# Kernel tuning notes

Hardware: AMD Instinct MI355X
Metric: run time of the kernel (lower is better)

The kernel has to match this reference:

```python
import jax, jax.numpy as jnp
import numpy as np

BN_EPS = 1e-5
CLAMP = 1e-4


def setup_inputs() -> dict:
    key = jax.random.key(0)
    ks = jax.random.split(key, 13)
    B, C, T, A = 32, 1536, 1000, 128
    s = 0.02  # keep conv pre-activations in a sane range
    return {
        "x": jax.random.normal(ks[0], (B, C, T), jnp.float32),
        "W1": jax.random.normal(ks[1], (A, 3 * C), jnp.float32) * s,
        "b1": jax.random.normal(ks[2], (A,), jnp.float32) * s,
        "g1": jax.random.uniform(ks[3], (A,), jnp.float32, 0.5, 1.5),
        "beta1": jax.random.normal(ks[4], (A,), jnp.float32) * 0.1,
        "rm1": jax.random.normal(ks[5], (A,), jnp.float32) * 0.1,
        "rv1": jax.random.uniform(ks[6], (A,), jnp.float32, 0.5, 1.5),
        "W2": jax.random.normal(ks[7], (C, A), jnp.float32) * s,
        "b2": jax.random.normal(ks[8], (C,), jnp.float32) * s,
        "g2": jax.random.uniform(ks[9], (C,), jnp.float32, 0.5, 1.5),
        "beta2": jax.random.normal(ks[10], (C,), jnp.float32) * 0.1,
        "rm2": jax.random.normal(ks[11], (C,), jnp.float32) * 0.1,
        "rv2": jax.random.uniform(ks[12], (C,), jnp.float32, 0.5, 1.5),
    }


def _bn(h, g, beta, rm, rv):
    # inference-mode BatchNorm1d over channel axis 1 of [B, C, T]
    inv = g / jnp.sqrt(rv + BN_EPS)
    return h * inv[None, :, None] + (beta - rm * inv)[None, :, None]


def reference(x, W1, b1, g1, beta1, rm1, rv1, W2, b2, g2, beta2, rm2, rv2):
    B, C, T = x.shape
    mean = jnp.mean(x, axis=2)                       # [B, C]
    var = jnp.var(x, axis=2, ddof=1)                 # unbiased, matches torch.var
    std = jnp.sqrt(jnp.clip(var, CLAMP, None))       # [B, C]
    # 1x1 conv over concat([x, mean.repeat(T), std.repeat(T)]) without
    # materializing the [B, 3C, T] tensor: split W1 into three channel blocks.
    Wx, Wm, Ws = W1[:, :C], W1[:, C:2 * C], W1[:, 2 * C:]
    h = jnp.einsum('oc,bct->bot', Wx, x)             # [B, A, T]
    h = h + (mean @ Wm.T + std @ Ws.T + b1)[:, :, None]
    h = jax.nn.relu(h)
    h = _bn(h, g1, beta1, rm1, rv1)
    h = jnp.tanh(h)
    h = jnp.einsum('oa,bat->bot', W2, h) + b2[None, :, None]  # [B, C, T]
    h = jax.nn.relu(h)
    h = _bn(h, g2, beta2, rm2, rv2)
    w = jax.nn.softmax(h, axis=2)                    # attention over time
    mu = jnp.sum(x * w, axis=2)                      # [B, C]
    sg = jnp.sqrt(jnp.clip(jnp.sum(x * x * w, axis=2) - mu * mu, CLAMP, None))
    return jnp.concatenate([mu, sg], axis=1)         # [B, 2C]
```

## Files before the change

### kernel.cpp

```cpp
#include <hip/hip_runtime.h>
#include <cmath>

#define BN_EPS 1e-5f
#define CLAMPV 1e-4f

static constexpr int B_ = 32, C_ = 1536, T_ = 1000, A_ = 128;
static constexpr int C3 = 3 * C_;
static constexpr int TP = 1024;
static constexpr int KS1 = C_ / 32;
static constexpr int KS2 = A_ / 32;
static constexpr int OM1 = A_ / 16;
static constexpr int OM2 = C_ / 16;

using bf16x8 = __attribute__((ext_vector_type(8))) short;
using f32x4  = __attribute__((ext_vector_type(4))) float;

#define MFMA(a, b, c) __builtin_amdgcn_mfma_f32_16x16x32_bf16(a, b, c, 0, 0, 0)

static constexpr size_t WT_OFF    = 0;
static constexpr size_t MEAN_OFF  = 393216;
static constexpr size_t STD_OFF   = MEAN_OFF + 49152;
static constexpr size_t BIASP_OFF = STD_OFF + 49152;
static constexpr size_t BIAS_OFF  = BIASP_OFF + 32768;
static constexpr size_t INV1_OFF  = BIAS_OFF + 4096;
static constexpr size_t SH1_OFF   = INV1_OFF + 128;
static constexpr size_t INV2_OFF  = SH1_OFF + 128;
static constexpr size_t SH2_OFF   = INV2_OFF + 1536;
static constexpr size_t WXH_OFF   = SH2_OFF + 1536;
static constexpr size_t WXL_OFF   = WXH_OFF + 98304;
static constexpr size_t W2H_OFF   = WXL_OFF + 98304;
static constexpr size_t W2L_OFF   = W2H_OFF + 98304;
static constexpr size_t HTP_OFF   = W2L_OFF + 98304;
static constexpr size_t HPART_OFF = HTP_OFF + 4194304;
static constexpr size_t SP_OFF    = HPART_OFF + 8388608;
static constexpr size_t PP_OFF    = SP_OFF + 393216;
static constexpr size_t QP_OFF    = PP_OFF + 393216;

__device__ __forceinline__ short f2bf(float v) {
  __bf16 b = (__bf16)v;
  return __builtin_bit_cast(short, b);
}
__device__ __forceinline__ float bf2f(short s) {
  unsigned int u = ((unsigned int)(unsigned short)s) << 16;
  return __builtin_bit_cast(float, u);
}

__global__ __launch_bounds__(256) void k_transpose(const float* __restrict__ W1,
                                                   float* __restrict__ WT) {
  __shared__ float tile[32][33];
  int c0 = blockIdx.x * 32;
  int o0 = blockIdx.y * 32;
  int tx = threadIdx.x, ty = threadIdx.y;
#pragma unroll
  for (int k = 0; k < 32; k += 8)
    tile[ty + k][tx] = W1[(size_t)(o0 + ty + k) * C3 + C_ + c0 + tx];
  __syncthreads();
#pragma unroll
  for (int k = 0; k < 32; k += 8)
    WT[(size_t)(c0 + ty + k) * A_ + o0 + tx] = tile[tx][ty + k];
}

__global__ __launch_bounds__(256) void k_stats(const float* __restrict__ x,
                                               float* __restrict__ mean,
                                               float* __restrict__ stdv) {
  int row  = blockIdx.x * 4 + (threadIdx.x >> 6);
  int lane = threadIdx.x & 63;
  const float2* xr2 = (const float2*)(x + (size_t)row * T_);
  float s1 = 0.f, s2 = 0.f;
#pragma unroll 4
  for (int j = lane; j < T_ / 2; j += 64) {
    float2 v = xr2[j];
    s1 += v.x + v.y;
    s2 += v.x * v.x + v.y * v.y;
  }
#pragma unroll
  for (int off = 32; off; off >>= 1) {
    s1 += __shfl_xor(s1, off);
    s2 += __shfl_xor(s2, off);
  }
  if (lane == 0) {
    float m   = s1 / T_;
    float var = (s2 - s1 * m) / (T_ - 1);
    mean[row] = m;
    stdv[row] = sqrtf(fmaxf(var, CLAMPV));
  }
}

__global__ void k_bn(const float* __restrict__ g1, const float* __restrict__ beta1,
                     const float* __restrict__ rm1, const float* __restrict__ rv1,
                     const float* __restrict__ g2, const float* __restrict__ beta2,
                     const float* __restrict__ rm2, const float* __restrict__ rv2,
                     float* inv1, float* sh1, float* inv2, float* sh2) {
  int i = blockIdx.x * 256 + threadIdx.x;
  if (i < A_) { float iv = g1[i] * rsqrtf(rv1[i] + BN_EPS); inv1[i] = iv; sh1[i] = beta1[i] - rm1[i] * iv; }
  if (i < C_) { float iv = g2[i] * rsqrtf(rv2[i] + BN_EPS); inv2[i] = iv; sh2[i] = beta2[i] - rm2[i] * iv; }
}

__global__ __launch_bounds__(256) void k_pack_w(const float* __restrict__ W1,
                                                const float* __restrict__ W2,
                                                unsigned short* __restrict__ WxH,
                                                unsigned short* __restrict__ WxL,
                                                unsigned short* __restrict__ W2H,
                                                unsigned short* __restrict__ W2L) {
  int id = blockIdx.x * 256 + threadIdx.x;
  if (id < OM1 * KS1 * 64) {
    int l = id & 63; int ks = (id >> 6) % KS1; int om = id / (64 * KS1);
    int o  = om * 16 + (l & 15);
    int c0 = ks * 32 + (l >> 4) * 8;
#pragma unroll
    for (int j = 0; j < 8; j++) {
      float v = W1[(size_t)o * C3 + c0 + j];
      short h = f2bf(v); float fh = bf2f(h); short lo = f2bf(v - fh);
      WxH[(size_t)id * 8 + j] = (unsigned short)h;
      WxL[(size_t)id * 8 + j] = (unsigned short)lo;
    }
  } else {
    int id2 = id - OM1 * KS1 * 64;
    int l = id2 & 63; int ks = (id2 >> 6) & 3; int om = id2 / (64 * KS2);
    int cr = om * 16 + (l & 15);
    int a0 = ks * 32 + (l >> 4) * 8;
#pragma unroll
    for (int j = 0; j < 8; j++) {
      float v = W2[(size_t)cr * A_ + a0 + j];
      short h = f2bf(v); float fh = bf2f(h); short lo = f2bf(v - fh);
      W2H[(size_t)id2 * 8 + j] = (unsigned short)h;
      W2L[(size_t)id2 * 8 + j] = (unsigned short)lo;
    }
  }
}

__global__ __launch_bounds__(256) void k_biasPart(const float* __restrict__ WT,
                                                  const float* __restrict__ mean,
                                                  const float* __restrict__ stdv,
                                                  float* __restrict__ biasPart) {
  __shared__ float sm[192], ss[192];
  __shared__ float red[2][128];
  int b = blockIdx.x, cg = blockIdx.y;
  int tix = threadIdx.x;
  if (tix < 192) {
    sm[tix] = mean[b * C_ + cg * 192 + tix];
    ss[tix] = stdv[b * C_ + cg * 192 + tix];
  }
  __syncthreads();
  int o = tix & 127, cs = tix >> 7;
  float acc = 0.f;
#pragma unroll 4
  for (int i = 0; i < 96; i++) {
    int c = cs * 96 + i;
    int cgl = cg * 192 + c;
    acc += sm[c] * WT[(size_t)cgl * A_ + o] + ss[c] * WT[(size_t)(C_ + cgl) * A_ + o];
  }
  red[cs][o] = acc;
  __syncthreads();
  if (tix < 128)
    biasPart[((size_t)cg * B_ + b) * A_ + tix] = red[0][tix] + red[1][tix];
}

__global__ void k_bias2(const float* __restrict__ b1, const float* __restrict__ biasPart,
                        float* __restrict__ bias1) {
  int b = blockIdx.x, o = threadIdx.x;
  float a = b1[o];
#pragma unroll
  for (int g = 0; g < 8; g++) a += biasPart[((size_t)g * B_ + b) * A_ + o];
  bias1[b * A_ + o] = a;
}

__global__ __launch_bounds__(256, 4) void k_gemm1(const float* __restrict__ x,
    const unsigned short* __restrict__ WxH, const unsigned short* __restrict__ WxL,
    float* __restrict__ hPart) {
  int b = blockIdx.x, tt = blockIdx.y, kc = blockIdx.z;
  int wid = threadIdx.x >> 6, l = threadIdx.x & 63;
  int wm = wid & 1, wn = wid >> 1;
  int lg = l >> 4, ll = l & 15;

  f32x4 acc[4][2];
#pragma unroll
  for (int mi = 0; mi < 4; mi++)
#pragma unroll
    for (int ns = 0; ns < 2; ns++) acc[mi][ns] = (f32x4){0.f, 0.f, 0.f, 0.f};

  const float* xb = x + (size_t)b * C_ * T_;
  int tbase = tt * 64 + wn * 32;
  int   tloc[2];
  float tmask[2];
#pragma unroll
  for (int ns = 0; ns < 2; ns++) {
    int t = tbase + ns * 16 + ll;
    tloc[ns]  = t < T_ ? t : T_ - 1;
    tmask[ns] = t < T_ ? 1.f : 0.f;
  }

  for (int ksl = 0; ksl < KS1 / 2; ksl++) {
    int ks = kc * (KS1 / 2) + ksl;
    bf16x8 ah[4], al[4];
#pragma unroll
    for (int mi = 0; mi < 4; mi++) {
      size_t fi = ((size_t)((wm * 4 + mi) * KS1 + ks) * 64 + l) * 8;
      ah[mi] = *(const bf16x8*)(WxH + fi);
      al[mi] = *(const bf16x8*)(WxL + fi);
    }
    int cg = ks * 32 + lg * 8;
    bf16x8 bh[2], bl[2];
#pragma unroll
    for (int ns = 0; ns < 2; ns++) {
      const float* xp = xb + tloc[ns];
      float m = tmask[ns];
#pragma unroll
      for (int j = 0; j < 8; j++) {
        float v = xp[(size_t)(cg + j) * T_] * m;
        short h = f2bf(v); float fh = bf2f(h); short lo = f2bf(v - fh);
        bh[ns][j] = h; bl[ns][j] = lo;
      }
    }
#pragma unroll
    for (int mi = 0; mi < 4; mi++)
#pragma unroll
      for (int ns = 0; ns < 2; ns++) {
        acc[mi][ns] = MFMA(ah[mi], bh[ns], acc[mi][ns]);
        acc[mi][ns] = MFMA(ah[mi], bl[ns], acc[mi][ns]);
        acc[mi][ns] = MFMA(al[mi], bh[ns], acc[mi][ns]);
      }
  }

#pragma unroll
  for (int mi = 0; mi < 4; mi++)
#pragma unroll
    for (int r = 0; r < 4; r++) {
      int o = wm * 64 + mi * 16 + lg * 4 + r;
#pragma unroll
      for (int ns = 0; ns < 2; ns++) {
        int t = tbase + ns * 16 + ll;
        hPart[(((size_t)kc * B_ + b) * A_ + o) * TP + t] = acc[mi][ns][r];
      }
    }
}

__global__ __launch_bounds__(256) void k_act(const float* __restrict__ hPart,
                                             const float* __restrict__ bias1,
                                             const float* __restrict__ inv1,
                                             const float* __restrict__ sh1,
                                             unsigned int* __restrict__ htP) {
  int bo = blockIdx.x;
  int t  = blockIdx.y * 256 + threadIdx.x;
  int b = bo >> 7, o = bo & 127;
  float v = hPart[(size_t)bo * TP + t] + hPart[((size_t)B_ * A_ + bo) * TP + t]
          + bias1[b * A_ + o];
  v = fmaxf(v, 0.f) * inv1[o] + sh1[o];
  float e  = __expf(2.f * v);
  float th = 1.f - 2.f / (e + 1.f);
  short h = f2bf(th); float fh = bf2f(h); short lo = f2bf(th - fh);
  htP[(size_t)bo * TP + t] = ((unsigned int)(unsigned short)h << 16) | (unsigned short)lo;
}

__global__ __launch_bounds__(512, 4) void k_pool(const float* __restrict__ x,
    const unsigned int* __restrict__ htP,
    const unsigned short* __restrict__ W2H, const unsigned short* __restrict__ W2L,
    const float* __restrict__ b2, const float* __restrict__ inv2, const float* __restrict__ sh2,
    float* __restrict__ SP, float* __restrict__ PP, float* __restrict__ QP) {
  int b = blockIdx.x, cb = blockIdx.y, th = blockIdx.z;
  int tix = threadIdx.x;
  int wid = tix >> 6, l = tix & 63;
  int wm = wid & 1, wt = wid >> 1;
  int lg = l >> 4, ll = l & 15;

  __shared__ float sb2[128], siv[128], ssh[128];
  __shared__ float rS[4][128], rP[4][128], rQ[4][128];
  if (tix < 128) {
    int c = cb * 128 + tix;
    sb2[tix] = b2[c]; siv[tix] = inv2[c]; ssh[tix] = sh2[c];
  }
  __syncthreads();

  f32x4 acc[4][2];
#pragma unroll
  for (int mi = 0; mi < 4; mi++)
#pragma unroll
    for (int ns = 0; ns < 2; ns++) acc[mi][ns] = (f32x4){0.f, 0.f, 0.f, 0.f};

  const unsigned int* hb = htP + (size_t)b * A_ * TP;
  int tb = th * 128 + wt * 32;

  for (int ks = 0; ks < KS2; ks++) {
    bf16x8 bh[2], bl[2];
    int ag = ks * 32 + lg * 8;
#pragma unroll
    for (int ns = 0; ns < 2; ns++) {
      int t = tb + ns * 16 + ll;
#pragma unroll
      for (int j = 0; j < 8; j++) {
        unsigned int v = hb[(size_t)(ag + j) * TP + t];
        bh[ns][j] = (short)(v >> 16);
        bl[ns][j] = (short)(v & 0xffffu);
      }
    }
#pragma unroll
    for (int mi = 0; mi < 4; mi++) {
      size_t fi = ((size_t)((cb * 8 + wm * 4 + mi) * KS2 + ks) * 64 + l) * 8;
      bf16x8 ah = *(const bf16x8*)(W2H + fi);
      bf16x8 al = *(const bf16x8*)(W2L + fi);
#pragma unroll
      for (int ns = 0; ns < 2; ns++) {
        acc[mi][ns] = MFMA(ah, bh[ns], acc[mi][ns]);
        acc[mi][ns] = MFMA(ah, bl[ns], acc[mi][ns]);
        acc[mi][ns] = MFMA(al, bh[ns], acc[mi][ns]);
      }
    }
  }

  const float* xb = x + (size_t)b * C_ * T_;
#pragma unroll
  for (int mi = 0; mi < 4; mi++) {
#pragma unroll
    for (int r = 0; r < 4; r++) {
      int cl = wm * 64 + mi * 16 + lg * 4 + r;
      float s = 0.f, p = 0.f, q = 0.f;
#pragma unroll
      for (int ns = 0; ns < 2; ns++) {
        int t = tb + ns * 16 + ll;
        float em = t < T_ ? 1.f : 0.f;
        int   te = t < T_ ? t : T_ - 1;
        float h2 = acc[mi][ns][r] + sb2[cl];
        float z  = fmaxf(h2, 0.f) * siv[cl] + ssh[cl];
        float e  = __expf(z) * em;
        float xv = xb[(size_t)(cb * 128 + cl) * T_ + te];
        s += e; p += e * xv; q += e * xv * xv;
      }
#pragma unroll
      for (int d = 1; d < 16; d <<= 1) {
        s += __shfl_xor(s, d);
        p += __shfl_xor(p, d);
        q += __shfl_xor(q, d);
      }
      if (ll == 0) { rS[wt][cl] = s; rP[wt][cl] = p; rQ[wt][cl] = q; }
    }
  }
  __syncthreads();
  if (tix < 128) {
    float S = rS[0][tix] + rS[1][tix] + rS[2][tix] + rS[3][tix];
    float P = rP[0][tix] + rP[1][tix] + rP[2][tix] + rP[3][tix];
    float Q = rQ[0][tix] + rQ[1][tix] + rQ[2][tix] + rQ[3][tix];
    size_t o = ((size_t)th * B_ + b) * C_ + cb * 128 + tix;
    SP[o] = S; PP[o] = P; QP[o] = Q;
  }
}

__global__ void k_finish(const float* __restrict__ SP, const float* __restrict__ PP,
                         const float* __restrict__ QP, float* __restrict__ out) {
  int i = blockIdx.x * 256 + threadIdx.x;
  if (i >= B_ * C_) return;
  int b = i / C_, c = i % C_;
  float S = 0.f, P = 0.f, Q = 0.f;
#pragma unroll
  for (int t8 = 0; t8 < 8; t8++) {
    size_t o = ((size_t)t8 * B_ + b) * C_ + c;
    S += SP[o]; P += PP[o]; Q += QP[o];
  }
  float mu  = P / S;
  float var = Q / S - mu * mu;
  out[(size_t)b * 2 * C_ + c]      = mu;
  out[(size_t)b * 2 * C_ + C_ + c] = sqrtf(fmaxf(var, CLAMPV));
}

extern "C" void kernel_launch(void* const* d_in, const int* in_sizes, int n_in,
                              void* d_out, int out_size, void* d_ws, size_t ws_size,
                              hipStream_t stream) {
  const float* x     = (const float*)d_in[0];
  const float* W1    = (const float*)d_in[1];
  const float* b1    = (const float*)d_in[2];
  const float* g1    = (const float*)d_in[3];
  const float* beta1 = (const float*)d_in[4];
  const float* rm1   = (const float*)d_in[5];
  const float* rv1   = (const float*)d_in[6];
  const float* W2    = (const float*)d_in[7];
  const float* b2    = (const float*)d_in[8];
  const float* g2    = (const float*)d_in[9];
  const float* beta2 = (const float*)d_in[10];
  const float* rm2   = (const float*)d_in[11];
  const float* rv2   = (const float*)d_in[12];

  float* ws     = (float*)d_ws;
  float* WT     = ws + WT_OFF;
  float* mean   = ws + MEAN_OFF;
  float* stdv   = ws + STD_OFF;
  float* biasP  = ws + BIASP_OFF;
  float* bias1  = ws + BIAS_OFF;
  float* inv1   = ws + INV1_OFF;
  float* sh1    = ws + SH1_OFF;
  float* inv2   = ws + INV2_OFF;
  float* sh2    = ws + SH2_OFF;
  unsigned short* WxH = (unsigned short*)(ws + WXH_OFF);
  unsigned short* WxL = (unsigned short*)(ws + WXL_OFF);
  unsigned short* W2H = (unsigned short*)(ws + W2H_OFF);
  unsigned short* W2L = (unsigned short*)(ws + W2L_OFF);
  unsigned int*   htP = (unsigned int*)(ws + HTP_OFF);
  float* hPart  = ws + HPART_OFF;
  float* SP = ws + SP_OFF;
  float* PP = ws + PP_OFF;
  float* QP = ws + QP_OFF;
  float* out = (float*)d_out;

  k_bn<<<dim3(6), 256, 0, stream>>>(g1, beta1, rm1, rv1, g2, beta2, rm2, rv2,
                                    inv1, sh1, inv2, sh2);
  k_transpose<<<dim3(96, 4), dim3(32, 8), 0, stream>>>(W1, WT);
  k_pack_w<<<dim3(192), 256, 0, stream>>>(W1, W2, WxH, WxL, W2H, W2L);
  k_stats<<<dim3(B_ * C_ / 4), 256, 0, stream>>>(x, mean, stdv);
  k_biasPart<<<dim3(B_, 8), 256, 0, stream>>>(WT, mean, stdv, biasP);
  k_bias2<<<dim3(B_), 128, 0, stream>>>(b1, biasP, bias1);
  k_gemm1<<<dim3(B_, 16, 2), 256, 0, stream>>>(x, WxH, WxL, hPart);
  k_act<<<dim3(B_ * A_, TP / 256), 256, 0, stream>>>(hPart, bias1, inv1, sh1, htP);
  k_pool<<<dim3(B_, 12, 8), 512, 0, stream>>>(x, htP, W2H, W2L, b2, inv2, sh2, SP, PP, QP);
  k_finish<<<dim3((B_ * C_ + 255) / 256), 256, 0, stream>>>(SP, PP, QP, out);
}
```

Measured before the change: 494.4 us.

## Drop activation low-part split and store hidden tensor time-major as bf16

The x and tanh activations now use a single bf16 part instead of a hi/lo split, which removes one of the three MFMAs per product in both GEMMs. The hidden buffers are moved to [b][t][a] layout, so gemm1 writes f32x4 vectors and k_pool reads contiguous bf16x8 operands instead of eight strided scalar loads. The intermediate activation buffer halves to 16-bit. The trade is lower precision on the activation side, which may move results relative to the reference.

Result: no change. 491.1 us (-0.7%).

```diff
diff --git a/kernel.cpp b/kernel.cpp
--- a/kernel.cpp
+++ b/kernel.cpp
@@ -10,7 +10,6 @@
 static constexpr int KS1 = C_ / 32;
 static constexpr int KS2 = A_ / 32;
 static constexpr int OM1 = A_ / 16;
-static constexpr int OM2 = C_ / 16;
 
 using bf16x8 = __attribute__((ext_vector_type(8))) short;
 using f32x4  = __attribute__((ext_vector_type(4))) float;
@@ -30,8 +29,8 @@
 static constexpr size_t WXL_OFF   = WXH_OFF + 98304;
 static constexpr size_t W2H_OFF   = WXL_OFF + 98304;
 static constexpr size_t W2L_OFF   = W2H_OFF + 98304;
-static constexpr size_t HTP_OFF   = W2L_OFF + 98304;
-static constexpr size_t HPART_OFF = HTP_OFF + 4194304;
+static constexpr size_t HTT_OFF   = W2L_OFF + 98304;
+static constexpr size_t HPART_OFF = HTT_OFF + 2097152;
 static constexpr size_t SP_OFF    = HPART_OFF + 8388608;
 static constexpr size_t PP_OFF    = SP_OFF + 393216;
 static constexpr size_t QP_OFF    = PP_OFF + 393216;
@@ -200,7 +199,7 @@
       al[mi] = *(const bf16x8*)(WxL + fi);
     }
     int cg = ks * 32 + lg * 8;
-    bf16x8 bh[2], bl[2];
+    bf16x8 bh[2];
 #pragma unroll
     for (int ns = 0; ns < 2; ns++) {
       const float* xp = xb + tloc[ns];
@@ -208,8 +207,7 @@
 #pragma unroll
       for (int j = 0; j < 8; j++) {
         float v = xp[(size_t)(cg + j) * T_] * m;
-        short h = f2bf(v); float fh = bf2f(h); short lo = f2bf(v - fh);
-        bh[ns][j] = h; bl[ns][j] = lo;
+        bh[ns][j] = f2bf(v);
       }
     }
 #pragma unroll
@@ -217,21 +215,18 @@
 #pragma unroll
       for (int ns = 0; ns < 2; ns++) {
         acc[mi][ns] = MFMA(ah[mi], bh[ns], acc[mi][ns]);
-        acc[mi][ns] = MFMA(ah[mi], bl[ns], acc[mi][ns]);
         acc[mi][ns] = MFMA(al[mi], bh[ns], acc[mi][ns]);
       }
   }
 
+  float* hp = hPart + ((size_t)kc * B_ + b) * TP * A_;
 #pragma unroll
   for (int mi = 0; mi < 4; mi++)
 #pragma unroll
-    for (int r = 0; r < 4; r++) {
-      int o = wm * 64 + mi * 16 + lg * 4 + r;
-#pragma unroll
-      for (int ns = 0; ns < 2; ns++) {
-        int t = tbase + ns * 16 + ll;
-        hPart[(((size_t)kc * B_ + b) * A_ + o) * TP + t] = acc[mi][ns][r];
-      }
+    for (int ns = 0; ns < 2; ns++) {
+      int t = tbase + ns * 16 + ll;
+      int o = wm * 64 + mi * 16 + lg * 4;
+      *(f32x4*)(hp + (size_t)t * A_ + o) = acc[mi][ns];
     }
 }
 
@@ -239,21 +234,20 @@
                                              const float* __restrict__ bias1,
                                              const float* __restrict__ inv1,
                                              const float* __restrict__ sh1,
-                                             unsigned int* __restrict__ htP) {
-  int bo = blockIdx.x;
-  int t  = blockIdx.y * 256 + threadIdx.x;
-  int b = bo >> 7, o = bo & 127;
-  float v = hPart[(size_t)bo * TP + t] + hPart[((size_t)B_ * A_ + bo) * TP + t]
-          + bias1[b * A_ + o];
-  v = fmaxf(v, 0.f) * inv1[o] + sh1[o];
+                                             unsigned short* __restrict__ htT) {
+  int b = blockIdx.x;
+  int t = blockIdx.y * 2 + (threadIdx.x >> 7);
+  int a = threadIdx.x & 127;
+  size_t i0 = ((size_t)b * TP + t) * A_ + a;
+  float v = hPart[i0] + hPart[(size_t)B_ * TP * A_ + i0] + bias1[b * A_ + a];
+  v = fmaxf(v, 0.f) * inv1[a] + sh1[a];
   float e  = __expf(2.f * v);
   float th = 1.f - 2.f / (e + 1.f);
-  short h = f2bf(th); float fh = bf2f(h); short lo = f2bf(th - fh);
-  htP[(size_t)bo * TP + t] = ((unsigned int)(unsigned short)h << 16) | (unsigned short)lo;
+  htT[i0] = (unsigned short)f2bf(th);
 }
 
 __global__ __launch_bounds__(512, 4) void k_pool(const float* __restrict__ x,
-    const unsigned int* __restrict__ htP,
+    const unsigned short* __restrict__ htT,
     const unsigned short* __restrict__ W2H, const unsigned short* __restrict__ W2L,
     const float* __restrict__ b2, const float* __restrict__ inv2, const float* __restrict__ sh2,
     float* __restrict__ SP, float* __restrict__ PP, float* __restrict__ QP) {
@@ -277,21 +271,16 @@
 #pragma unroll
     for (int ns = 0; ns < 2; ns++) acc[mi][ns] = (f32x4){0.f, 0.f, 0.f, 0.f};
 
-  const unsigned int* hb = htP + (size_t)b * A_ * TP;
+  const unsigned short* hb = htT + (size_t)b * TP * A_;
   int tb = th * 128 + wt * 32;
 
   for (int ks = 0; ks < KS2; ks++) {
-    bf16x8 bh[2], bl[2];
     int ag = ks * 32 + lg * 8;
+    bf16x8 bh[2];
 #pragma unroll
     for (int ns = 0; ns < 2; ns++) {
       int t = tb + ns * 16 + ll;
-#pragma unroll
-      for (int j = 0; j < 8; j++) {
-        unsigned int v = hb[(size_t)(ag + j) * TP + t];
-        bh[ns][j] = (short)(v >> 16);
-        bl[ns][j] = (short)(v & 0xffffu);
-      }
+      bh[ns] = *(const bf16x8*)(hb + (size_t)t * A_ + ag);
     }
 #pragma unroll
     for (int mi = 0; mi < 4; mi++) {
@@ -301,7 +290,6 @@
 #pragma unroll
       for (int ns = 0; ns < 2; ns++) {
         acc[mi][ns] = MFMA(ah, bh[ns], acc[mi][ns]);
-        acc[mi][ns] = MFMA(ah, bl[ns], acc[mi][ns]);
         acc[mi][ns] = MFMA(al, bh[ns], acc[mi][ns]);
       }
     }
@@ -392,7 +380,7 @@
   unsigned short* WxL = (unsigned short*)(ws + WXL_OFF);
   unsigned short* W2H = (unsigned short*)(ws + W2H_OFF);
   unsigned short* W2L = (unsigned short*)(ws + W2L_OFF);
-  unsigned int*   htP = (unsigned int*)(ws + HTP_OFF);
+  unsigned short* htT = (unsigned short*)(ws + HTT_OFF);
   float* hPart  = ws + HPART_OFF;
   float* SP = ws + SP_OFF;
   float* PP = ws + PP_OFF;
@@ -407,7 +395,7 @@
   k_biasPart<<<dim3(B_, 8), 256, 0, stream>>>(WT, mean, stdv, biasP);
   k_bias2<<<dim3(B_), 128, 0, stream>>>(b1, biasP, bias1);
   k_gemm1<<<dim3(B_, 16, 2), 256, 0, stream>>>(x, WxH, WxL, hPart);
-  k_act<<<dim3(B_ * A_, TP / 256), 256, 0, stream>>>(hPart, bias1, inv1, sh1, htP);
-  k_pool<<<dim3(B_, 12, 8), 512, 0, stream>>>(x, htP, W2H, W2L, b2, inv2, sh2, SP, PP, QP);
+  k_act<<<dim3(B_, TP / 2), 256, 0, stream>>>(hPart, bias1, inv1, sh1, htT);
+  k_pool<<<dim3(B_, 12, 8), 512, 0, stream>>>(x, htT, W2H, W2L, b2, inv2, sh2, SP, PP, QP);
   k_finish<<<dim3((B_ * C_ + 255) / 256), 256, 0, stream>>>(SP, PP, QP, out);
 }
```
